# Kernel optimization log

Measured on AMD Instinct MI355X. Metric: run time of the kernel, lower is better.

The kernel has to match this reference:

```python
import jax, jax.numpy as jnp
import numpy as np

HEADS = 24
KV_HEADS = 6
HEAD_DIM = 64


def _partial_rope(x, cos, sin):
    # x: [B, H, S, head_dim]; cos/sin: [S, rot_dim]; rotate first rot_dim dims
    rot_dim = cos.shape[-1]
    x_rot, x_pass = x[..., :rot_dim], x[..., rot_dim:]
    half = rot_dim // 2
    # use_real_unbind_dim=-2: reshape (..., 2, half) then unbind -> first/second half
    x_real, x_imag = x_rot[..., :half], x_rot[..., half:]
    x_rotated = jnp.concatenate([-x_imag, x_real], axis=-1)
    out = x_rot * cos[None, None] + x_rotated * sin[None, None]
    return jnp.concatenate([out, x_pass], axis=-1)


def setup_inputs() -> dict:
    key = jax.random.key(0)
    ks = jax.random.split(key, 8)
    B, S, D = 2, 2048, 1536
    kv_dim = KV_HEADS * HEAD_DIM
    rot_dim = 32
    hidden_states = jax.random.normal(ks[0], (B, S, D), dtype=jnp.float32)
    # realistic rotary cos/sin from inv-freq angles
    pos = jnp.arange(S, dtype=jnp.float32)
    inv_freq = 1.0 / (10000.0 ** (jnp.arange(0, rot_dim, 2, dtype=jnp.float32) / rot_dim))
    ang = pos[:, None] * inv_freq[None, :]  # [S, rot_dim//2]
    ang = jnp.concatenate([ang, ang], axis=-1)  # [S, rot_dim]
    cos, sin = jnp.cos(ang), jnp.sin(ang)
    Wq = jax.random.normal(ks[1], (D, D), dtype=jnp.float32) * 0.02
    Wk = jax.random.normal(ks[2], (D, kv_dim), dtype=jnp.float32) * 0.02
    Wv = jax.random.normal(ks[3], (D, kv_dim), dtype=jnp.float32) * 0.02
    Wo = jax.random.normal(ks[4], (D, D), dtype=jnp.float32) * 0.02
    bo = jnp.zeros((D,), dtype=jnp.float32)
    return {"hidden_states": hidden_states, "cos": cos, "sin": sin,
            "Wq": Wq, "Wk": Wk, "Wv": Wv, "Wo": Wo, "bo": bo}


def reference(hidden_states, cos, sin, Wq, Wk, Wv, Wo, bo):
    B, S, D = hidden_states.shape
    residual = hidden_states
    q = hidden_states @ Wq  # [B,S,D]
    k = hidden_states @ Wk  # [B,S,kv_dim]
    v = hidden_states @ Wv
    q = q.reshape(B, S, HEADS, HEAD_DIM).transpose(0, 2, 1, 3)       # [B,H,S,d]
    k = k.reshape(B, S, KV_HEADS, HEAD_DIM).transpose(0, 2, 1, 3)    # [B,Hkv,S,d]
    v = v.reshape(B, S, KV_HEADS, HEAD_DIM).transpose(0, 2, 1, 3)
    rep = HEADS // KV_HEADS
    k = jnp.repeat(k, rep, axis=1)  # GQA repeat_interleave -> [B,H,S,d]
    v = jnp.repeat(v, rep, axis=1)
    # partial RoPE on query and key (self-attention)
    q = _partial_rope(q, cos, sin)
    k = _partial_rope(k, cos, sin)
    scale = 1.0 / jnp.sqrt(jnp.float32(HEAD_DIM))
    scores = jnp.einsum('bhqd,bhkd->bhqk', q, k) * scale
    probs = jax.nn.softmax(scores, axis=-1)
    out = jnp.einsum('bhqk,bhkd->bhqd', probs, v)
    out = out.transpose(0, 2, 1, 3).reshape(B, S, D)
    out = out @ Wo + bo
    return out + residual
```

## Files before the change

kernel.cpp:

```cpp
#include <hip/hip_runtime.h>

#define HEADS 24
#define KVH   6
#define HD    64
#define BB    2
#define SS    2048
#define DD    1536
#define KVD   384
#define QKD   1920
#define MM    4096

typedef unsigned short ushort_t;
typedef __attribute__((ext_vector_type(8))) short short8;
typedef __attribute__((ext_vector_type(4))) short short4v;
typedef __attribute__((ext_vector_type(4))) float f32x4;

__device__ __forceinline__ ushort_t f2bf(float f) {
    union { float f; unsigned u; } v; v.f = f;
    return (ushort_t)((v.u + 0x8000u) >> 16);
}
__device__ __forceinline__ unsigned pk2(float a, float b) {
    union { float f; unsigned u; } x, y; x.f = a; y.f = b;
    return ((x.u + 0x8000u) >> 16) | (((y.u + 0x8000u) >> 16) << 16);
}
__device__ __forceinline__ unsigned pk2t(float a, float b) {
    union { float f; unsigned u; } x, y; x.f = a; y.f = b;
    return (x.u >> 16) | (y.u & 0xFFFF0000u);
}
__device__ __forceinline__ float fexp2(float s) {
    float t = fmaf(s, 8388608.0f, 1065055420.0f);
    union { int i; float f; } v; v.i = (int)t;
    return v.f;
}
__device__ __forceinline__ short8 lds_frag8(const ushort_t* p) {
    short4v lo = *(const short4v*)p;
    short4v hi = *(const short4v*)(p + 4);
    return __builtin_shufflevector(lo, hi, 0, 1, 2, 3, 4, 5, 6, 7);
}
__device__ __forceinline__ void glds16(const void* g, void* l) {
    __builtin_amdgcn_global_load_lds(
        (const __attribute__((address_space(1))) void*)g,
        (__attribute__((address_space(3))) void*)l, 16, 0, 0);
}

__device__ __forceinline__ void tconv_body(const float* __restrict__ in,
                                           ushort_t* __restrict__ out,
                                           int R, int C, int cb, int rb)
{
    __shared__ ushort_t tile[32][33];
    const int tx = threadIdx.x & 31, ty = threadIdx.x >> 5;
    const int c0 = cb * 32, r0 = rb * 32;
#pragma unroll
    for (int i = 0; i < 4; ++i)
        tile[ty + i * 8][tx] = f2bf(in[(size_t)(r0 + ty + i * 8) * C + c0 + tx]);
    __syncthreads();
#pragma unroll
    for (int i = 0; i < 4; ++i)
        out[(size_t)(c0 + ty + i * 8) * R + r0 + tx] = tile[tx][ty + i * 8];
}

#define NCVT (MM * DD / 4 / 256)
__global__ __launch_bounds__(256) void k_prep(const float* __restrict__ HS,
                                              const float* __restrict__ Wq,
                                              const float* __restrict__ Wk,
                                              const float* __restrict__ Wv,
                                              const float* __restrict__ Wo,
                                              ushort_t* __restrict__ Xbf,
                                              ushort_t* __restrict__ Wqt,
                                              ushort_t* __restrict__ Wkt,
                                              ushort_t* __restrict__ Wvt,
                                              ushort_t* __restrict__ Wot)
{
    int bid = blockIdx.x;
    if (bid < NCVT) {
        int i = bid * 256 + threadIdx.x;
        float4 v = ((const float4*)HS)[i];
        uint2 o = { pk2(v.x, v.y), pk2(v.z, v.w) };
        ((uint2*)Xbf)[i] = o;
        return;
    }
    bid -= NCVT;
    if (bid < 2304) { tconv_body(Wq, Wqt, DD, DD,  bid % 48, bid / 48); return; }
    bid -= 2304;
    if (bid < 576)  { tconv_body(Wk, Wkt, DD, KVD, bid % 12, bid / 12); return; }
    bid -= 576;
    if (bid < 576)  { tconv_body(Wv, Wvt, DD, KVD, bid % 12, bid / 12); return; }
    bid -= 576;
    tconv_body(Wo, Wot, DD, DD, bid % 48, bid / 48);
}

__global__ __launch_bounds__(256) void k_proj(const ushort_t* __restrict__ Xbf,
                                              const ushort_t* __restrict__ Wqt,
                                              const ushort_t* __restrict__ Wkt,
                                              const ushort_t* __restrict__ Wvt,
                                              const float* __restrict__ cosb,
                                              const float* __restrict__ sinb,
                                              ushort_t* __restrict__ QKVb,
                                              ushort_t* __restrict__ VT)
{
    __shared__ ushort_t As[128][32];
    __shared__ ushort_t Bs[128][32];
    const int t = threadIdx.x, lane = t & 63, wave = t >> 6;
    const int n16 = lane & 15, quad = lane >> 4;
    const int wr = wave >> 1, wc = wave & 1;
    const int srow = lane >> 2;
    const int scol = (lane & 3) * 8;

    if (blockIdx.x < 480) {
        const int nt = blockIdx.x % 15;
        const int n0 = nt * 128;
        const int m0 = (blockIdx.x / 15) * 128;
        const ushort_t* Bt; int nl, isq;
        if (nt < 12) { Bt = Wqt; nl = n0;      isq = 1; }
        else         { Bt = Wkt; nl = n0 - DD; isq = 0; }

        const size_t aoff0 = (size_t)(m0 + wave * 16 + srow) * DD + scol;
        const size_t aoff1 = (size_t)(m0 + (wave + 4) * 16 + srow) * DD + scol;
        const size_t boff0 = (size_t)(nl + wave * 16 + srow) * DD + scol;
        const size_t boff1 = (size_t)(nl + (wave + 4) * 16 + srow) * DD + scol;
        ushort_t* lA0 = &As[wave * 16][0];
        ushort_t* lA1 = &As[(wave + 4) * 16][0];
        ushort_t* lB0 = &Bs[wave * 16][0];
        ushort_t* lB1 = &Bs[(wave + 4) * 16][0];

        f32x4 acc[4][4] = {};
        for (int k0 = 0; k0 < DD; k0 += 32) {
            __syncthreads();
            glds16(Xbf + aoff0 + k0, lA0);
            glds16(Xbf + aoff1 + k0, lA1);
            glds16(Bt  + boff0 + k0, lB0);
            glds16(Bt  + boff1 + k0, lB1);
            __syncthreads();
            short8 af[4], bf8[4];
#pragma unroll
            for (int i = 0; i < 4; ++i) af[i]  = *(const short8*)&As[wr * 64 + i * 16 + n16][quad * 8];
#pragma unroll
            for (int j = 0; j < 4; ++j) bf8[j] = *(const short8*)&Bs[wc * 64 + j * 16 + n16][quad * 8];
#pragma unroll
            for (int i = 0; i < 4; ++i)
#pragma unroll
                for (int j = 0; j < 4; ++j)
                    acc[i][j] = __builtin_amdgcn_mfma_f32_16x16x32_bf16(af[i], bf8[j], acc[i][j], 0, 0, 0);
        }

        const float QSC = 0.18033688011112042f;
#pragma unroll
        for (int i = 0; i < 4; ++i) {
#pragma unroll
            for (int r = 0; r < 4; ++r) {
                const int row = m0 + wr * 64 + i * 16 + quad * 4 + r;
                ushort_t* outp = QKVb + (size_t)row * QKD + n0 + wc * 64 + n16;
                float v0 = acc[i][0][r], v1 = acc[i][1][r];
                float v2 = acc[i][2][r], v3 = acc[i][3][r];
                {
                    const int s = row & (SS - 1);
                    float c0 = cosb[s * 32 + n16],      s0 = sinb[s * 32 + n16];
                    float c1 = cosb[s * 32 + 16 + n16], s1 = sinb[s * 32 + 16 + n16];
                    float nr = v0 * c0 - v1 * s0;
                    float ni = v1 * c1 + v0 * s1;
                    v0 = nr; v1 = ni;
                }
                if (isq) { v0 *= QSC; v1 *= QSC; v2 *= QSC; v3 *= QSC; }
                outp[0]  = f2bf(v0);
                outp[16] = f2bf(v1);
                outp[32] = f2bf(v2);
                outp[48] = f2bf(v3);
            }
        }
    } else {
        const int vb = blockIdx.x - 480;
        const int n0 = (vb & 31) * 128;
        const int m0 = (vb >> 5) * 64;

        const size_t aoff  = (size_t)(m0 + wave * 16 + srow) * DD + scol;
        const size_t boff0 = (size_t)(n0 + wave * 32 + srow) * DD + scol;
        const size_t boff1 = boff0 + (size_t)16 * DD;
        ushort_t* lA  = &As[wave * 16][0];
        ushort_t* lB0 = &Bs[wave * 32][0];
        ushort_t* lB1 = &Bs[wave * 32 + 16][0];

        f32x4 acc[2][4] = {};
        for (int k0 = 0; k0 < DD; k0 += 32) {
            __syncthreads();
            glds16(Wvt + aoff  + k0, lA);
            glds16(Xbf + boff0 + k0, lB0);
            glds16(Xbf + boff1 + k0, lB1);
            __syncthreads();
            short8 af[2], bf8[4];
#pragma unroll
            for (int i = 0; i < 2; ++i) af[i]  = *(const short8*)&As[wr * 32 + i * 16 + n16][quad * 8];
#pragma unroll
            for (int j = 0; j < 4; ++j) bf8[j] = *(const short8*)&Bs[wc * 64 + j * 16 + n16][quad * 8];
#pragma unroll
            for (int i = 0; i < 2; ++i)
#pragma unroll
                for (int j = 0; j < 4; ++j)
                    acc[i][j] = __builtin_amdgcn_mfma_f32_16x16x32_bf16(af[i], bf8[j], acc[i][j], 0, 0, 0);
        }

        const int b = n0 >> 11;
        const int s0 = 8 * (n16 >> 2) + 2 * (n16 & 3);
#pragma unroll
        for (int i = 0; i < 2; ++i)
#pragma unroll
            for (int r = 0; r < 4; ++r) {
                const int c = m0 + wr * 32 + i * 16 + quad * 4 + r;
                ushort_t* op = VT + ((size_t)b * KVD + c) * SS +
                               (n0 & (SS - 1)) + wc * 64 + s0;
                *(unsigned*)op        = pk2(acc[i][0][r], acc[i][1][r]);
                *(unsigned*)(op + 32) = pk2(acc[i][2][r], acc[i][3][r]);
            }
    }
}

__global__ __launch_bounds__(256) void k_attn(const ushort_t* __restrict__ QKVb,
                                              const ushort_t* __restrict__ VT,
                                              ushort_t* __restrict__ AOb)
{
    __shared__ __align__(16) ushort_t Ks[64][76];
    __shared__ __align__(16) ushort_t Vs[64][76];

    const int t    = threadIdx.x;
    const int wave = t >> 6;
    const int quad = (t >> 4) & 3;
    const int n16  = t & 15;
    const int q0   = blockIdx.x * 128;
    const int h    = blockIdx.y;
    const int b    = blockIdx.z;
    const int kh   = h >> 2;

    const int sr = t >> 2;
    const int sc = (t & 3) * 8;
    const int vc = (t & 3) * 16;

    short8 qf[2][2];
#pragma unroll
    for (int m = 0; m < 2; ++m)
#pragma unroll
        for (int kc = 0; kc < 2; ++kc)
            qf[m][kc] = *(const short8*)(QKVb +
                (size_t)(b * SS + q0 + wave * 32 + m * 16 + n16) * QKD +
                h * HD + kc * 32 + quad * 8);

    float l_p[2] = {};
    f32x4 acc_o[2][4] = {};

    const ushort_t* Kbase = QKVb + (size_t)(b * SS) * QKD + DD + kh * HD;
    const ushort_t* Vbase = VT + ((size_t)b * KVD + kh * 64) * SS;

    for (int kt = 0; kt < SS / 64; ++kt) {
        const int k0 = kt * 64;
        __syncthreads();
        {
            const ushort_t* Kg = Kbase + (size_t)(k0 + sr) * QKD + sc;
            uint4 kv0 = *(const uint4*)(Kg);
            uint4 kv1 = *(const uint4*)(Kg + 32);
            *(uint2*)&Ks[sr][sc]      = make_uint2(kv0.x, kv0.y);
            *(uint2*)&Ks[sr][sc + 4]  = make_uint2(kv0.z, kv0.w);
            *(uint2*)&Ks[sr][sc + 32] = make_uint2(kv1.x, kv1.y);
            *(uint2*)&Ks[sr][sc + 36] = make_uint2(kv1.z, kv1.w);
            const ushort_t* Vg = Vbase + (size_t)sr * SS + k0 + vc;
            uint4 vv0 = *(const uint4*)(Vg);
            uint4 vv1 = *(const uint4*)(Vg + 8);
            *(uint2*)&Vs[sr][vc]      = make_uint2(vv0.x, vv0.y);
            *(uint2*)&Vs[sr][vc + 4]  = make_uint2(vv0.z, vv0.w);
            *(uint2*)&Vs[sr][vc + 8]  = make_uint2(vv1.x, vv1.y);
            *(uint2*)&Vs[sr][vc + 12] = make_uint2(vv1.z, vv1.w);
        }
        __syncthreads();

        f32x4 sT[2][4] = {};
#pragma unroll
        for (int kc = 0; kc < 2; ++kc) {
            short8 bf[4];
#pragma unroll
            for (int jj = 0; jj < 4; ++jj)
                bf[jj] = lds_frag8(&Ks[jj * 16 + n16][kc * 32 + quad * 8]);
#pragma unroll
            for (int m = 0; m < 2; ++m)
#pragma unroll
                for (int jj = 0; jj < 4; ++jj)
                    sT[m][jj] = __builtin_amdgcn_mfma_f32_16x16x32_bf16(
                        bf[jj], qf[m][kc], sT[m][jj], 0, 0, 0);
        }

        union PB { unsigned w[4]; short8 v; };
        PB pb[2][2];
#pragma unroll
        for (int m = 0; m < 2; ++m) {
#pragma unroll
            for (int w = 0; w < 4; ++w) {
                float p0 = fexp2(sT[m][0][w]);
                float p1 = fexp2(sT[m][1][w]);
                float p2 = fexp2(sT[m][2][w]);
                float p3 = fexp2(sT[m][3][w]);
                pb[m][0].w[w] = pk2t(p0, p1);
                pb[m][1].w[w] = pk2t(p2, p3);
                l_p[m] += (p0 + p1) + (p2 + p3);
            }
        }

#pragma unroll
        for (int kc = 0; kc < 2; ++kc) {
            short8 vb[4];
#pragma unroll
            for (int dd = 0; dd < 4; ++dd)
                vb[dd] = lds_frag8(&Vs[dd * 16 + n16][kc * 32 + quad * 8]);
#pragma unroll
            for (int m = 0; m < 2; ++m)
#pragma unroll
                for (int dd = 0; dd < 4; ++dd)
                    acc_o[m][dd] = __builtin_amdgcn_mfma_f32_16x16x32_bf16(
                        vb[dd], pb[m][kc].v, acc_o[m][dd], 0, 0, 0);
        }
    }

#pragma unroll
    for (int m = 0; m < 2; ++m) {
        float s = l_p[m];
        s += __shfl_xor(s, 16);
        s += __shfl_xor(s, 32);
        const float inv = 1.0f / s;
        const int q = q0 + wave * 32 + m * 16 + n16;
        ushort_t* op = AOb + (size_t)(b * SS + q) * DD + h * HD + quad * 4;
#pragma unroll
        for (int dd = 0; dd < 4; ++dd) {
            uint2 o = { pk2(acc_o[m][dd][0] * inv, acc_o[m][dd][1] * inv),
                        pk2(acc_o[m][dd][2] * inv, acc_o[m][dd][3] * inv) };
            *(uint2*)(op + dd * 16) = o;
        }
    }
}

__global__ __launch_bounds__(256) void k_out_mfma(const ushort_t* __restrict__ AOb,
                                                  const ushort_t* __restrict__ Wot,
                                                  const float* __restrict__ bo,
                                                  const float* __restrict__ HS,
                                                  float* __restrict__ out)
{
    __shared__ ushort_t As[64][32];
    __shared__ ushort_t Bs[128][32];
    const int t = threadIdx.x, lane = t & 63, wave = t >> 6;
    const int n16 = lane & 15, quad = lane >> 4;
    const int wr = wave >> 1, wc = wave & 1;
    const int n0 = blockIdx.x * 128;
    const int m0 = blockIdx.y * 64;

    const int srow = lane >> 2;
    const int scol = (lane & 3) * 8;
    const size_t aoff  = (size_t)(m0 + wave * 16 + srow) * DD + scol;
    const size_t boff0 = (size_t)(n0 + wave * 32 + srow) * DD + scol;
    const size_t boff1 = boff0 + (size_t)16 * DD;
    ushort_t* lA  = &As[wave * 16][0];
    ushort_t* lB0 = &Bs[wave * 32][0];
    ushort_t* lB1 = &Bs[wave * 32 + 16][0];

    f32x4 acc[2][4] = {};
    for (int k0 = 0; k0 < DD; k0 += 32) {
        __syncthreads();
        glds16(AOb + aoff  + k0, lA);
        glds16(Wot + boff0 + k0, lB0);
        glds16(Wot + boff1 + k0, lB1);
        __syncthreads();
        short8 af[2], bf8[4];
#pragma unroll
        for (int i = 0; i < 2; ++i) af[i]  = *(const short8*)&As[wr * 32 + i * 16 + n16][quad * 8];
#pragma unroll
        for (int j = 0; j < 4; ++j) bf8[j] = *(const short8*)&Bs[wc * 64 + j * 16 + n16][quad * 8];
#pragma unroll
        for (int i = 0; i < 2; ++i)
#pragma unroll
            for (int j = 0; j < 4; ++j)
                acc[i][j] = __builtin_amdgcn_mfma_f32_16x16x32_bf16(af[i], bf8[j], acc[i][j], 0, 0, 0);
    }

    const int colb = n0 + wc * 64 + n16;
    float bo4[4];
#pragma unroll
    for (int j = 0; j < 4; ++j) bo4[j] = bo[colb + j * 16];
#pragma unroll
    for (int i = 0; i < 2; ++i) {
#pragma unroll
        for (int r = 0; r < 4; ++r) {
            const int row = m0 + wr * 32 + i * 16 + quad * 4 + r;
            float* op = out + (size_t)row * DD + colb;
            const float* hp = HS + (size_t)row * DD + colb;
#pragma unroll
            for (int j = 0; j < 4; ++j)
                op[j * 16] = acc[i][j][r] + bo4[j] + hp[j * 16];
        }
    }
}

extern "C" void kernel_launch(void* const* d_in, const int* in_sizes, int n_in,
                              void* d_out, int out_size, void* d_ws, size_t ws_size,
                              hipStream_t stream)
{
    const float* HS   = (const float*)d_in[0];
    const float* cosb = (const float*)d_in[1];
    const float* sinb = (const float*)d_in[2];
    const float* Wq   = (const float*)d_in[3];
    const float* Wk   = (const float*)d_in[4];
    const float* Wv   = (const float*)d_in[5];
    const float* Wo   = (const float*)d_in[6];
    const float* bo   = (const float*)d_in[7];
    float* out = (float*)d_out;

    ushort_t* Xbf  = (ushort_t*)d_ws;
    ushort_t* QKVb = Xbf  + (size_t)MM * DD;
    ushort_t* AOb  = QKVb + (size_t)MM * QKD;
    ushort_t* Wqt  = AOb  + (size_t)MM * DD;
    ushort_t* Wkt  = Wqt  + (size_t)DD * DD;
    ushort_t* Wvt  = Wkt  + (size_t)KVD * DD;
    ushort_t* Wot  = Wvt  + (size_t)KVD * DD;
    ushort_t* VT   = Wot  + (size_t)DD * DD;

    const int nprep = NCVT + 2304 + 576 + 576 + 2304;
    k_prep    <<<dim3(nprep), 256, 0, stream>>>(HS, Wq, Wk, Wv, Wo,
                                                Xbf, Wqt, Wkt, Wvt, Wot);
    k_proj    <<<dim3(480 + 192), 256, 0, stream>>>(Xbf, Wqt, Wkt, Wvt,
                                                    cosb, sinb, QKVb, VT);
    k_attn    <<<dim3(SS / 128, HEADS, BB), 256, 0, stream>>>(QKVb, VT, AOb);
    k_out_mfma<<<dim3(DD / 128, MM / 64),   256, 0, stream>>>(AOb, Wot, bo, HS, out);
}
```

Measured before the change: 259.0 us.

## Double-buffer K/V tiles in attention kernel with register prefetch

The attention kernel now holds two LDS buffers for K and V and prefetches the next-next tile into registers while the current tile is computed. After each tile's compute, the prefetched registers go into the other buffer, so the loop needs one barrier per iteration instead of two and global load latency can overlap with MFMA work. In exchange it doubles the LDS footprint and keeps extra registers live, which may lower occupancy.

```diff
diff --git a/kernel.cpp b/kernel.cpp
--- a/kernel.cpp
+++ b/kernel.cpp
@@ -217,8 +217,8 @@
                                               const ushort_t* __restrict__ VT,
                                               ushort_t* __restrict__ AOb)
 {
-    __shared__ __align__(16) ushort_t Ks[64][76];
-    __shared__ __align__(16) ushort_t Vs[64][76];
+    __shared__ __align__(16) ushort_t Ks[2][64][76];
+    __shared__ __align__(16) ushort_t Vs[2][64][76];
 
     const int t    = threadIdx.x;
     const int wave = t >> 6;
@@ -248,26 +248,38 @@
     const ushort_t* Kbase = QKVb + (size_t)(b * SS) * QKD + DD + kh * HD;
     const ushort_t* Vbase = VT + ((size_t)b * KVD + kh * 64) * SS;
 
-    for (int kt = 0; kt < SS / 64; ++kt) {
-        const int k0 = kt * 64;
-        __syncthreads();
-        {
-            const ushort_t* Kg = Kbase + (size_t)(k0 + sr) * QKD + sc;
-            uint4 kv0 = *(const uint4*)(Kg);
-            uint4 kv1 = *(const uint4*)(Kg + 32);
-            *(uint2*)&Ks[sr][sc]      = make_uint2(kv0.x, kv0.y);
-            *(uint2*)&Ks[sr][sc + 4]  = make_uint2(kv0.z, kv0.w);
-            *(uint2*)&Ks[sr][sc + 32] = make_uint2(kv1.x, kv1.y);
-            *(uint2*)&Ks[sr][sc + 36] = make_uint2(kv1.z, kv1.w);
-            const ushort_t* Vg = Vbase + (size_t)sr * SS + k0 + vc;
-            uint4 vv0 = *(const uint4*)(Vg);
-            uint4 vv1 = *(const uint4*)(Vg + 8);
-            *(uint2*)&Vs[sr][vc]      = make_uint2(vv0.x, vv0.y);
-            *(uint2*)&Vs[sr][vc + 4]  = make_uint2(vv0.z, vv0.w);
-            *(uint2*)&Vs[sr][vc + 8]  = make_uint2(vv1.x, vv1.y);
-            *(uint2*)&Vs[sr][vc + 12] = make_uint2(vv1.z, vv1.w);
-        }
-        __syncthreads();
+    uint4 kv0, kv1, vv0, vv1;
+
+#define LOAD_TILE(K0) do {                                                  \
+        const ushort_t* Kg = Kbase + (size_t)((K0) + sr) * QKD + sc;        \
+        kv0 = *(const uint4*)(Kg);                                          \
+        kv1 = *(const uint4*)(Kg + 32);                                     \
+        const ushort_t* Vg = Vbase + (size_t)sr * SS + (K0) + vc;           \
+        vv0 = *(const uint4*)(Vg);                                          \
+        vv1 = *(const uint4*)(Vg + 8);                                      \
+    } while (0)
+
+#define WRITE_BUF(BI) do {                                                  \
+        *(uint2*)&Ks[BI][sr][sc]      = make_uint2(kv0.x, kv0.y);           \
+        *(uint2*)&Ks[BI][sr][sc + 4]  = make_uint2(kv0.z, kv0.w);           \
+        *(uint2*)&Ks[BI][sr][sc + 32] = make_uint2(kv1.x, kv1.y);           \
+        *(uint2*)&Ks[BI][sr][sc + 36] = make_uint2(kv1.z, kv1.w);           \
+        *(uint2*)&Vs[BI][sr][vc]      = make_uint2(vv0.x, vv0.y);           \
+        *(uint2*)&Vs[BI][sr][vc + 4]  = make_uint2(vv0.z, vv0.w);           \
+        *(uint2*)&Vs[BI][sr][vc + 8]  = make_uint2(vv1.x, vv1.y);           \
+        *(uint2*)&Vs[BI][sr][vc + 12] = make_uint2(vv1.z, vv1.w);           \
+    } while (0)
+
+    LOAD_TILE(0);
+    WRITE_BUF(0);
+    LOAD_TILE(64);
+    __syncthreads();
+
+    const int NT = SS / 64;
+    for (int kt = 0; kt < NT; ++kt) {
+        const int cur = kt & 1;
+        const ushort_t (*Kc)[76] = Ks[cur];
+        const ushort_t (*Vc)[76] = Vs[cur];
 
         f32x4 sT[2][4] = {};
 #pragma unroll
@@ -275,7 +287,7 @@
             short8 bf[4];
 #pragma unroll
             for (int jj = 0; jj < 4; ++jj)
-                bf[jj] = lds_frag8(&Ks[jj * 16 + n16][kc * 32 + quad * 8]);
+                bf[jj] = lds_frag8(&Kc[jj * 16 + n16][kc * 32 + quad * 8]);
 #pragma unroll
             for (int m = 0; m < 2; ++m)
 #pragma unroll
@@ -305,7 +317,7 @@
             short8 vb[4];
 #pragma unroll
             for (int dd = 0; dd < 4; ++dd)
-                vb[dd] = lds_frag8(&Vs[dd * 16 + n16][kc * 32 + quad * 8]);
+                vb[dd] = lds_frag8(&Vc[dd * 16 + n16][kc * 32 + quad * 8]);
 #pragma unroll
             for (int m = 0; m < 2; ++m)
 #pragma unroll
@@ -313,7 +325,16 @@
                     acc_o[m][dd] = __builtin_amdgcn_mfma_f32_16x16x32_bf16(
                         vb[dd], pb[m][kc].v, acc_o[m][dd], 0, 0, 0);
         }
-    }
+
+        if (kt + 1 < NT) {
+            WRITE_BUF(cur ^ 1);
+            if (kt + 2 < NT)
+                LOAD_TILE((kt + 2) * 64);
+            __syncthreads();
+        }
+    }
+#undef LOAD_TILE
+#undef WRITE_BUF
 
 #pragma unroll
     for (int m = 0; m < 2; ++m) {
```

New measurement: 251.6 us. -2.8%, faster.

## Load attention K/V MFMA fragments directly from global memory, dropping LDS staging

Applied to the files above, without the earlier changes.

The attention kernel no longer stages K and V tiles through shared memory with two barriers per iteration. Each wave now loads its MFMA operand fragments straight from global memory through per-lane pointers. This removes the LDS round trip and the syncthreads, and launch bounds now request three blocks per CU. The cost is that every wave reloads the same K/V data (four waves per block), so more traffic falls on L1/L2, and there is no explicit prefetch to hide global latency. The bf16 truncating pack also switches to a single v_perm.

```diff
diff --git a/kernel.cpp b/kernel.cpp
--- a/kernel.cpp
+++ b/kernel.cpp
@@ -12,7 +12,6 @@
 
 typedef unsigned short ushort_t;
 typedef __attribute__((ext_vector_type(8))) short short8;
-typedef __attribute__((ext_vector_type(4))) short short4v;
 typedef __attribute__((ext_vector_type(4))) float f32x4;
 
 __device__ __forceinline__ ushort_t f2bf(float f) {
@@ -25,17 +24,12 @@
 }
 __device__ __forceinline__ unsigned pk2t(float a, float b) {
     union { float f; unsigned u; } x, y; x.f = a; y.f = b;
-    return (x.u >> 16) | (y.u & 0xFFFF0000u);
+    return __builtin_amdgcn_perm(y.u, x.u, 0x07060302);
 }
 __device__ __forceinline__ float fexp2(float s) {
     float t = fmaf(s, 8388608.0f, 1065055420.0f);
     union { int i; float f; } v; v.i = (int)t;
     return v.f;
-}
-__device__ __forceinline__ short8 lds_frag8(const ushort_t* p) {
-    short4v lo = *(const short4v*)p;
-    short4v hi = *(const short4v*)(p + 4);
-    return __builtin_shufflevector(lo, hi, 0, 1, 2, 3, 4, 5, 6, 7);
 }
 __device__ __forceinline__ void glds16(const void* g, void* l) {
     __builtin_amdgcn_global_load_lds(
@@ -213,13 +207,10 @@
     }
 }
 
-__global__ __launch_bounds__(256) void k_attn(const ushort_t* __restrict__ QKVb,
-                                              const ushort_t* __restrict__ VT,
-                                              ushort_t* __restrict__ AOb)
-{
-    __shared__ __align__(16) ushort_t Ks[64][76];
-    __shared__ __align__(16) ushort_t Vs[64][76];
-
+__global__ __launch_bounds__(256, 3) void k_attn(const ushort_t* __restrict__ QKVb,
+                                                 const ushort_t* __restrict__ VT,
+                                                 ushort_t* __restrict__ AOb)
+{
     const int t    = threadIdx.x;
     const int wave = t >> 6;
     const int quad = (t >> 4) & 3;
@@ -229,10 +220,6 @@
     const int b    = blockIdx.z;
     const int kh   = h >> 2;
 
-    const int sr = t >> 2;
-    const int sc = (t & 3) * 8;
-    const int vc = (t & 3) * 16;
-
     short8 qf[2][2];
 #pragma unroll
     for (int m = 0; m < 2; ++m)
@@ -242,47 +229,43 @@
                 (size_t)(b * SS + q0 + wave * 32 + m * 16 + n16) * QKD +
                 h * HD + kc * 32 + quad * 8);
 
+    const ushort_t* kp[4];
+#pragma unroll
+    for (int jj = 0; jj < 4; ++jj)
+        kp[jj] = QKVb + (size_t)(b * SS + jj * 16 + n16) * QKD +
+                 DD + kh * HD + quad * 8;
+    const ushort_t* vp[4];
+#pragma unroll
+    for (int dd = 0; dd < 4; ++dd)
+        vp[dd] = VT + ((size_t)b * KVD + kh * 64 + dd * 16 + n16) * SS + quad * 8;
+
     float l_p[2] = {};
     f32x4 acc_o[2][4] = {};
 
-    const ushort_t* Kbase = QKVb + (size_t)(b * SS) * QKD + DD + kh * HD;
-    const ushort_t* Vbase = VT + ((size_t)b * KVD + kh * 64) * SS;
-
     for (int kt = 0; kt < SS / 64; ++kt) {
-        const int k0 = kt * 64;
-        __syncthreads();
-        {
-            const ushort_t* Kg = Kbase + (size_t)(k0 + sr) * QKD + sc;
-            uint4 kv0 = *(const uint4*)(Kg);
-            uint4 kv1 = *(const uint4*)(Kg + 32);
-            *(uint2*)&Ks[sr][sc]      = make_uint2(kv0.x, kv0.y);
-            *(uint2*)&Ks[sr][sc + 4]  = make_uint2(kv0.z, kv0.w);
-            *(uint2*)&Ks[sr][sc + 32] = make_uint2(kv1.x, kv1.y);
-            *(uint2*)&Ks[sr][sc + 36] = make_uint2(kv1.z, kv1.w);
-            const ushort_t* Vg = Vbase + (size_t)sr * SS + k0 + vc;
-            uint4 vv0 = *(const uint4*)(Vg);
-            uint4 vv1 = *(const uint4*)(Vg + 8);
-            *(uint2*)&Vs[sr][vc]      = make_uint2(vv0.x, vv0.y);
-            *(uint2*)&Vs[sr][vc + 4]  = make_uint2(vv0.z, vv0.w);
-            *(uint2*)&Vs[sr][vc + 8]  = make_uint2(vv1.x, vv1.y);
-            *(uint2*)&Vs[sr][vc + 12] = make_uint2(vv1.z, vv1.w);
-        }
-        __syncthreads();
+        short8 kf[4][2], vf[4][2];
+#pragma unroll
+        for (int jj = 0; jj < 4; ++jj) {
+            kf[jj][0] = *(const short8*)(kp[jj]);
+            kf[jj][1] = *(const short8*)(kp[jj] + 32);
+            kp[jj] += 64 * QKD;
+        }
+#pragma unroll
+        for (int dd = 0; dd < 4; ++dd) {
+            vf[dd][0] = *(const short8*)(vp[dd]);
+            vf[dd][1] = *(const short8*)(vp[dd] + 32);
+            vp[dd] += 64;
+        }
 
         f32x4 sT[2][4] = {};
 #pragma unroll
-        for (int kc = 0; kc < 2; ++kc) {
-            short8 bf[4];
-#pragma unroll
-            for (int jj = 0; jj < 4; ++jj)
-                bf[jj] = lds_frag8(&Ks[jj * 16 + n16][kc * 32 + quad * 8]);
+        for (int kc = 0; kc < 2; ++kc)
 #pragma unroll
             for (int m = 0; m < 2; ++m)
 #pragma unroll
                 for (int jj = 0; jj < 4; ++jj)
                     sT[m][jj] = __builtin_amdgcn_mfma_f32_16x16x32_bf16(
-                        bf[jj], qf[m][kc], sT[m][jj], 0, 0, 0);
-        }
+                        kf[jj][kc], qf[m][kc], sT[m][jj], 0, 0, 0);
 
         union PB { unsigned w[4]; short8 v; };
         PB pb[2][2];
@@ -301,18 +284,13 @@
         }
 
 #pragma unroll
-        for (int kc = 0; kc < 2; ++kc) {
-            short8 vb[4];
-#pragma unroll
-            for (int dd = 0; dd < 4; ++dd)
-                vb[dd] = lds_frag8(&Vs[dd * 16 + n16][kc * 32 + quad * 8]);
+        for (int kc = 0; kc < 2; ++kc)
 #pragma unroll
             for (int m = 0; m < 2; ++m)
 #pragma unroll
                 for (int dd = 0; dd < 4; ++dd)
                     acc_o[m][dd] = __builtin_amdgcn_mfma_f32_16x16x32_bf16(
-                        vb[dd], pb[m][kc].v, acc_o[m][dd], 0, 0, 0);
-        }
+                        vf[dd][kc], pb[m][kc].v, acc_o[m][dd], 0, 0, 0);
     }
 
 #pragma unroll
```

New measurement: 359.0 us. +38.7%, slower.
